# Kernel tuning notes

Hardware: AMD Instinct MI355X
Metric: run time of the kernel (lower is better)

Reference implementation:

```python
import jax, jax.numpy as jnp
import numpy as np

B, T, D, H, G = 256, 1024, 32, 64, 4 * 64  # batch, seq, input, hidden, gates


def setup_inputs() -> dict:
    key = jax.random.key(0)
    ks = jax.random.split(key, 12)
    s = 1.0 / np.sqrt(H)  # PyTorch LSTM default init scale
    return {
        "x": jax.random.normal(ks[0], (B, T, D), dtype=jnp.float32),
        "w_ih_l0": jax.random.normal(ks[1], (G, D), dtype=jnp.float32) * s,
        "w_hh_l0": jax.random.normal(ks[2], (G, H), dtype=jnp.float32) * s,
        "b_ih_l0": jax.random.normal(ks[3], (G,), dtype=jnp.float32) * s,
        "b_hh_l0": jax.random.normal(ks[4], (G,), dtype=jnp.float32) * s,
        "w_ih_l1": jax.random.normal(ks[5], (G, H), dtype=jnp.float32) * s,
        "w_hh_l1": jax.random.normal(ks[6], (G, H), dtype=jnp.float32) * s,
        "b_ih_l1": jax.random.normal(ks[7], (G,), dtype=jnp.float32) * s,
        "b_hh_l1": jax.random.normal(ks[8], (G,), dtype=jnp.float32) * s,
        "w_fc": jax.random.normal(ks[9], (1, H), dtype=jnp.float32) * s,
        "b_fc": jax.random.normal(ks[10], (1,), dtype=jnp.float32) * s,
    }


def _lstm_layer(x, w_ih, w_hh, b_ih, b_hh):
    """x: [B, T, Din] -> h_seq [B, T, H]. PyTorch gate order (i, f, g, o)."""
    # Precompute input contribution for all timesteps in one GEMM.
    gx = jnp.einsum('btd,gd->btg', x, w_ih) + b_ih + b_hh  # [B, T, 4H]
    gx = jnp.swapaxes(gx, 0, 1)  # [T, B, 4H] for scan over time
    h0 = jnp.zeros((x.shape[0], H), dtype=x.dtype)
    c0 = jnp.zeros((x.shape[0], H), dtype=x.dtype)

    def step(carry, g_t):
        h, c = carry
        g = g_t + h @ w_hh.T  # [B, 4H]
        i, f, gg, o = jnp.split(g, 4, axis=-1)
        i = jax.nn.sigmoid(i)
        f = jax.nn.sigmoid(f)
        gg = jnp.tanh(gg)
        o = jax.nn.sigmoid(o)
        c = f * c + i * gg
        h = o * jnp.tanh(c)
        return (h, c), h

    _, h_seq = jax.lax.scan(step, (h0, c0), gx)  # h_seq: [T, B, H]
    return jnp.swapaxes(h_seq, 0, 1)  # [B, T, H]


def reference(x, w_ih_l0, w_hh_l0, b_ih_l0, b_hh_l0,
              w_ih_l1, w_hh_l1, b_ih_l1, b_hh_l1, w_fc, b_fc):
    h1 = _lstm_layer(x, w_ih_l0, w_hh_l0, b_ih_l0, b_hh_l0)
    h2 = _lstm_layer(h1, w_ih_l1, w_hh_l1, b_ih_l1, b_hh_l1)
    last = h2[:, -1, :]  # [B, H]
    logits = last @ w_fc.T + b_fc  # [B, 1]
    return jax.nn.sigmoid(logits)
```

## Files before the change

kernel.cpp:

```cpp
#include <hip/hip_runtime.h>

#define TT 1024
#define DD 32
#define HH 64

typedef __fp16 h2v __attribute__((ext_vector_type(2)));
typedef _Float16 f16x8 __attribute__((ext_vector_type(8)));
typedef float f32x4 __attribute__((ext_vector_type(4)));

struct __attribute__((aligned(16))) H4 { h2v p[4]; };

__device__ __forceinline__ h2v pk(float a, float b) {
    return __builtin_amdgcn_cvt_pkrtz(a, b);
}
__device__ __forceinline__ float fsig(float x) {
    float e = __builtin_amdgcn_exp2f(-1.4426950408889634f * x);
    return __builtin_amdgcn_rcpf(1.0f + e);
}
__device__ __forceinline__ float ftanh(float x) {
    float e = __builtin_amdgcn_exp2f(2.885390081777927f * x);
    return 1.0f - 2.0f * __builtin_amdgcn_rcpf(1.0f + e);
}
__device__ __forceinline__ float pick4(f32x4 c, bool s0, bool s1) {
    float lo = s0 ? c[1] : c[0];
    float hi = s0 ? c[3] : c[2];
    return s1 ? hi : lo;
}
__device__ __forceinline__ f16x8 load_afrag(const float* p) {
    float4 f0 = *(const float4*)p;
    float4 f1 = *(const float4*)(p + 4);
    H4 t;
    t.p[0] = pk(f0.x, f0.y); t.p[1] = pk(f0.z, f0.w);
    t.p[2] = pk(f1.x, f1.y); t.p[3] = pk(f1.z, f1.w);
    return __builtin_bit_cast(f16x8, t);
}
#define MFMA16(A, B, C) __builtin_amdgcn_mfma_f32_16x16x32_f16(A, B, C, 0, 0, 0)

__global__ __launch_bounds__(512) void lstm2_b4(
    const float* __restrict__ x,
    const float* __restrict__ w_ih_l0, const float* __restrict__ w_hh_l0,
    const float* __restrict__ b_ih_l0, const float* __restrict__ b_hh_l0,
    const float* __restrict__ w_ih_l1, const float* __restrict__ w_hh_l1,
    const float* __restrict__ b_ih_l1, const float* __restrict__ b_hh_l1,
    const float* __restrict__ w_fc,   const float* __restrict__ b_fc,
    float* __restrict__ out)
{
    const int bbase = blockIdx.x * 4;
    const int tid  = threadIdx.x;
    const int wave = tid >> 6;
    const int lane = tid & 63;
    const bool isL1 = wave < 4;
    const int js   = wave & 3;
    const int quad = lane >> 4;
    const int bb   = lane & 3;
    const int rsel = (lane >> 2) & 3;
    const int jj   = js*16 + quad*4 + rsel;
    const int mrow = lane & 15;

    __shared__ __attribute__((aligned(16))) __fp16 buf[1280];

    {
        int* bi = (int*)buf;
        bi[tid] = 0;
        if (tid < 128) bi[512 + tid] = 0;
    }

    f16x8 A[16];
    float bs0, bs1, bs2, bs3;
    if (isL1) {
        #pragma unroll
        for (int q = 0; q < 4; ++q) {
            const int g = q*64 + js*16 + mrow;
            A[q*3 + 0] = load_afrag(w_ih_l0 + (size_t)g*DD + quad*8);
            A[q*3 + 1] = load_afrag(w_hh_l0 + (size_t)g*HH + quad*8);
            A[q*3 + 2] = load_afrag(w_hh_l0 + (size_t)g*HH + 32 + quad*8);
        }
        bs0 = b_ih_l0[0*64 + jj] + b_hh_l0[0*64 + jj];
        bs1 = b_ih_l0[1*64 + jj] + b_hh_l0[1*64 + jj];
        bs2 = b_ih_l0[2*64 + jj] + b_hh_l0[2*64 + jj];
        bs3 = b_ih_l0[3*64 + jj] + b_hh_l0[3*64 + jj];
    } else {
        #pragma unroll
        for (int q = 0; q < 4; ++q) {
            const int g = q*64 + js*16 + mrow;
            A[q*4 + 0] = load_afrag(w_ih_l1 + (size_t)g*HH + quad*8);
            A[q*4 + 1] = load_afrag(w_ih_l1 + (size_t)g*HH + 32 + quad*8);
            A[q*4 + 2] = load_afrag(w_hh_l1 + (size_t)g*HH + quad*8);
            A[q*4 + 3] = load_afrag(w_hh_l1 + (size_t)g*HH + 32 + quad*8);
        }
        bs0 = b_ih_l1[0*64 + jj] + b_hh_l1[0*64 + jj];
        bs1 = b_ih_l1[1*64 + jj] + b_hh_l1[1*64 + jj];
        bs2 = b_ih_l1[2*64 + jj] + b_hh_l1[2*64 + jj];
        bs3 = b_ih_l1[3*64 + jj] + b_hh_l1[3*64 + jj];
    }

    const int roff = (bb*4 + quad)*8;
    const int cw   = (isL1 ? 1 : 3) + (jj >> 5);
    const int woff = ((cw*4 + bb)*4 + ((jj & 31) >> 3))*8 + (jj & 7);

    const float* xg = x + (size_t)(bbase + (lane >> 4)) * (TT*DD) + (lane & 15)*2;
    const int sdw = ((lane >> 4)*4 + ((lane & 15) >> 2))*4 + ((lane & 15) & 3);
    float2 xv1 = {0.f, 0.f}, xv2 = {0.f, 0.f};

    __syncthreads();
    if (wave == 7) {
        float2 v0 = *(const float2*)xg;
        ((int*)buf)[sdw] = __builtin_bit_cast(int, pk(v0.x, v0.y));
        xv1 = *(const float2*)(xg + DD);
        xv2 = *(const float2*)(xg + 2*DD);
    }
    __syncthreads();

    const bool s0 = (rsel & 1) != 0;
    const bool s1 = (rsel & 2) != 0;
    float cst = 0.0f;

    for (int t = 0; t <= TT; ++t) {
        const int p = t & 1;
        const __fp16* bc = buf + p*640;
        __fp16* bn = buf + (p ^ 1)*640;
        if (isL1) {
            if (t < TT) {
                f16x8 B0 = *(const f16x8*)(bc + 0*128 + roff);
                f16x8 B1 = *(const f16x8*)(bc + 1*128 + roff);
                f16x8 B2 = *(const f16x8*)(bc + 2*128 + roff);

                f32x4 Z = {0.f, 0.f, 0.f, 0.f};
                f32x4 C0 = Z, C1 = Z, C2 = Z, C3 = Z;
                C0 = MFMA16(A[0], B0, C0); C0 = MFMA16(A[1],  B1, C0); C0 = MFMA16(A[2],  B2, C0);
                C1 = MFMA16(A[3], B0, C1); C1 = MFMA16(A[4],  B1, C1); C1 = MFMA16(A[5],  B2, C1);
                C2 = MFMA16(A[6], B0, C2); C2 = MFMA16(A[7],  B1, C2); C2 = MFMA16(A[8],  B2, C2);
                C3 = MFMA16(A[9], B0, C3); C3 = MFMA16(A[10], B1, C3); C3 = MFMA16(A[11], B2, C3);

                float Si = pick4(C0, s0, s1) + bs0;
                float Sf = pick4(C1, s0, s1) + bs1;
                float Sg = pick4(C2, s0, s1) + bs2;
                float So = pick4(C3, s0, s1) + bs3;

                float ii = fsig(Si), ff = fsig(Sf), oo = fsig(So);
                float gg = ftanh(Sg);
                cst = ff * cst + ii * gg;
                float hv = oo * ftanh(cst);
                bn[woff] = (__fp16)hv;
            }
        } else {
            if (wave == 7 && t < TT) {
                ((int*)bn)[sdw] = __builtin_bit_cast(int, pk(xv1.x, xv1.y));
                xv1 = xv2;
                const int tl = (t + 3 < TT) ? (t + 3) : (TT - 1);
                xv2 = *(const float2*)(xg + (size_t)tl*DD);
            }
            if (t > 0) {
                f16x8 B1 = *(const f16x8*)(bc + 1*128 + roff);
                f16x8 B2 = *(const f16x8*)(bc + 2*128 + roff);
                f16x8 B3 = *(const f16x8*)(bc + 3*128 + roff);
                f16x8 B4 = *(const f16x8*)(bc + 4*128 + roff);

                f32x4 Z = {0.f, 0.f, 0.f, 0.f};
                f32x4 C0 = Z, C1 = Z, C2 = Z, C3 = Z;
                C0 = MFMA16(A[0],  B1, C0); C0 = MFMA16(A[1],  B2, C0);
                C0 = MFMA16(A[2],  B3, C0); C0 = MFMA16(A[3],  B4, C0);
                C1 = MFMA16(A[4],  B1, C1); C1 = MFMA16(A[5],  B2, C1);
                C1 = MFMA16(A[6],  B3, C1); C1 = MFMA16(A[7],  B4, C1);
                C2 = MFMA16(A[8],  B1, C2); C2 = MFMA16(A[9],  B2, C2);
                C2 = MFMA16(A[10], B3, C2); C2 = MFMA16(A[11], B4, C2);
                C3 = MFMA16(A[12], B1, C3); C3 = MFMA16(A[13], B2, C3);
                C3 = MFMA16(A[14], B3, C3); C3 = MFMA16(A[15], B4, C3);

                float Si = pick4(C0, s0, s1) + bs0;
                float Sf = pick4(C1, s0, s1) + bs1;
                float Sg = pick4(C2, s0, s1) + bs2;
                float So = pick4(C3, s0, s1) + bs3;

                float ii = fsig(Si), ff = fsig(Sf), oo = fsig(So);
                float gg = ftanh(Sg);
                cst = ff * cst + ii * gg;
                float hv = oo * ftanh(cst);
                bn[woff] = (__fp16)hv;
            }
        }
        __syncthreads();
    }

    if (wave == 0) {
        const int jg = lane >> 2;
        float s = 0.f;
        #pragma unroll
        for (int u2 = 0; u2 < 4; ++u2) {
            const int j = jg*4 + u2;
            float hval = (float)buf[640 + (((3 + (j >> 5))*4 + bb)*4 + ((j & 31) >> 3))*8 + (j & 7)];
            s += hval * w_fc[j];
        }
        s += __shfl_xor(s, 4);
        s += __shfl_xor(s, 8);
        s += __shfl_xor(s, 16);
        s += __shfl_xor(s, 32);
        if (lane < 4) out[bbase + lane] = fsig(s + b_fc[0]);
    }
}

extern "C" void kernel_launch(void* const* d_in, const int* in_sizes, int n_in,
                              void* d_out, int out_size, void* d_ws, size_t ws_size,
                              hipStream_t stream) {
    lstm2_b4<<<dim3(64), dim3(512), 0, stream>>>(
        (const float*)d_in[0],
        (const float*)d_in[1], (const float*)d_in[2],
        (const float*)d_in[3], (const float*)d_in[4],
        (const float*)d_in[5], (const float*)d_in[6],
        (const float*)d_in[7], (const float*)d_in[8],
        (const float*)d_in[9], (const float*)d_in[10],
        (float*)d_out);
}
```

Measured before the change: 545.4 us.

## Feed x fragments straight from registers and split MFMA accumulation chains

Each layer-0 wave now loads its own x fragment from global memory into registers, with three timesteps prefetched, and packs it straight into the MFMA B operand. This drops the staging of x through shared memory by wave 7 and shrinks the LDS buffer. The dependent MFMA chains are split into two independent accumulators that are summed afterwards, to expose more instruction-level parallelism on the serial critical path. The per-step __syncthreads is replaced by an inline-asm LDS wait plus s_barrier, which avoids waiting on outstanding global loads. The cost is redundant global loads across the four layer-0 waves and extra registers.

```diff
diff --git a/kernel.cpp b/kernel.cpp
--- a/kernel.cpp
+++ b/kernel.cpp
@@ -20,23 +20,27 @@
 __device__ __forceinline__ float ftanh(float x) {
     float e = __builtin_amdgcn_exp2f(2.885390081777927f * x);
     return 1.0f - 2.0f * __builtin_amdgcn_rcpf(1.0f + e);
+}
+__device__ __forceinline__ void bar_lds() {
+    asm volatile("s_waitcnt lgkmcnt(0)\n\ts_barrier" ::: "memory");
 }
 __device__ __forceinline__ float pick4(f32x4 c, bool s0, bool s1) {
     float lo = s0 ? c[1] : c[0];
     float hi = s0 ? c[3] : c[2];
     return s1 ? hi : lo;
 }
+__device__ __forceinline__ f16x8 packx(float4 a, float4 b) {
+    H4 t;
+    t.p[0] = pk(a.x, a.y); t.p[1] = pk(a.z, a.w);
+    t.p[2] = pk(b.x, b.y); t.p[3] = pk(b.z, b.w);
+    return __builtin_bit_cast(f16x8, t);
+}
 __device__ __forceinline__ f16x8 load_afrag(const float* p) {
-    float4 f0 = *(const float4*)p;
-    float4 f1 = *(const float4*)(p + 4);
-    H4 t;
-    t.p[0] = pk(f0.x, f0.y); t.p[1] = pk(f0.z, f0.w);
-    t.p[2] = pk(f1.x, f1.y); t.p[3] = pk(f1.z, f1.w);
-    return __builtin_bit_cast(f16x8, t);
+    return packx(*(const float4*)p, *(const float4*)(p + 4));
 }
 #define MFMA16(A, B, C) __builtin_amdgcn_mfma_f32_16x16x32_f16(A, B, C, 0, 0, 0)
 
-__global__ __launch_bounds__(512) void lstm2_b4(
+__global__ __launch_bounds__(512) void lstm2_b4v2(
     const float* __restrict__ x,
     const float* __restrict__ w_ih_l0, const float* __restrict__ w_hh_l0,
     const float* __restrict__ b_ih_l0, const float* __restrict__ b_hh_l0,
@@ -57,13 +61,8 @@
     const int jj   = js*16 + quad*4 + rsel;
     const int mrow = lane & 15;
 
-    __shared__ __attribute__((aligned(16))) __fp16 buf[1280];
-
-    {
-        int* bi = (int*)buf;
-        bi[tid] = 0;
-        if (tid < 128) bi[512 + tid] = 0;
-    }
+    __shared__ __attribute__((aligned(16))) __fp16 buf[1024];
+    ((int*)buf)[tid] = 0;
 
     f16x8 A[16];
     float bs0, bs1, bs2, bs3;
@@ -95,47 +94,56 @@
     }
 
     const int roff = (bb*4 + quad)*8;
-    const int cw   = (isL1 ? 1 : 3) + (jj >> 5);
+    const int cw   = (isL1 ? 0 : 2) + (jj >> 5);
     const int woff = ((cw*4 + bb)*4 + ((jj & 31) >> 3))*8 + (jj & 7);
 
-    const float* xg = x + (size_t)(bbase + (lane >> 4)) * (TT*DD) + (lane & 15)*2;
-    const int sdw = ((lane >> 4)*4 + ((lane & 15) >> 2))*4 + ((lane & 15) & 3);
-    float2 xv1 = {0.f, 0.f}, xv2 = {0.f, 0.f};
-
-    __syncthreads();
-    if (wave == 7) {
-        float2 v0 = *(const float2*)xg;
-        ((int*)buf)[sdw] = __builtin_bit_cast(int, pk(v0.x, v0.y));
-        xv1 = *(const float2*)(xg + DD);
-        xv2 = *(const float2*)(xg + 2*DD);
-    }
+    const float* xg = x + (size_t)(bbase + bb) * (TT*DD) + quad*8;
+    float4 r0a, r0b, r1a, r1b, r2a, r2b;
+    if (isL1) {
+        r0a = *(const float4*)(xg);          r0b = *(const float4*)(xg + 4);
+        r1a = *(const float4*)(xg + DD);     r1b = *(const float4*)(xg + DD + 4);
+        r2a = *(const float4*)(xg + 2*DD);   r2b = *(const float4*)(xg + 2*DD + 4);
+    }
+
     __syncthreads();
 
     const bool s0 = (rsel & 1) != 0;
     const bool s1 = (rsel & 2) != 0;
     float cst = 0.0f;
+    const f32x4 Z = {0.f, 0.f, 0.f, 0.f};
 
     for (int t = 0; t <= TT; ++t) {
         const int p = t & 1;
-        const __fp16* bc = buf + p*640;
-        __fp16* bn = buf + (p ^ 1)*640;
+        const __fp16* bc = buf + p*512;
+        __fp16* bn = buf + (p ^ 1)*512;
         if (isL1) {
             if (t < TT) {
-                f16x8 B0 = *(const f16x8*)(bc + 0*128 + roff);
-                f16x8 B1 = *(const f16x8*)(bc + 1*128 + roff);
-                f16x8 B2 = *(const f16x8*)(bc + 2*128 + roff);
-
-                f32x4 Z = {0.f, 0.f, 0.f, 0.f};
-                f32x4 C0 = Z, C1 = Z, C2 = Z, C3 = Z;
-                C0 = MFMA16(A[0], B0, C0); C0 = MFMA16(A[1],  B1, C0); C0 = MFMA16(A[2],  B2, C0);
-                C1 = MFMA16(A[3], B0, C1); C1 = MFMA16(A[4],  B1, C1); C1 = MFMA16(A[5],  B2, C1);
-                C2 = MFMA16(A[6], B0, C2); C2 = MFMA16(A[7],  B1, C2); C2 = MFMA16(A[8],  B2, C2);
-                C3 = MFMA16(A[9], B0, C3); C3 = MFMA16(A[10], B1, C3); C3 = MFMA16(A[11], B2, C3);
-
-                float Si = pick4(C0, s0, s1) + bs0;
-                float Sf = pick4(C1, s0, s1) + bs1;
-                float Sg = pick4(C2, s0, s1) + bs2;
-                float So = pick4(C3, s0, s1) + bs3;
+                f16x8 Bx = packx(r0a, r0b);
+                r0a = r1a; r0b = r1b; r1a = r2a; r1b = r2b;
+                const int tl = (t + 3 < TT) ? (t + 3) : (TT - 1);
+                r2a = *(const float4*)(xg + (size_t)tl*DD);
+                r2b = *(const float4*)(xg + (size_t)tl*DD + 4);
+
+                f16x8 B1 = *(const f16x8*)(bc + 0*128 + roff);
+                f16x8 B2 = *(const f16x8*)(bc + 1*128 + roff);
+
+                f32x4 C0 = MFMA16(A[0], Bx, Z);
+                f32x4 C1 = MFMA16(A[3], Bx, Z);
+                f32x4 C2 = MFMA16(A[6], Bx, Z);
+                f32x4 C3 = MFMA16(A[9], Bx, Z);
+                C0 = MFMA16(A[1],  B1, C0);
+                C1 = MFMA16(A[4],  B1, C1);
+                C2 = MFMA16(A[7],  B1, C2);
+                C3 = MFMA16(A[10], B1, C3);
+                f32x4 D0 = MFMA16(A[2],  B2, Z);
+                f32x4 D1 = MFMA16(A[5],  B2, Z);
+                f32x4 D2 = MFMA16(A[8],  B2, Z);
+                f32x4 D3 = MFMA16(A[11], B2, Z);
+
+                float Si = pick4(C0, s0, s1) + pick4(D0, s0, s1) + bs0;
+                float Sf = pick4(C1, s0, s1) + pick4(D1, s0, s1) + bs1;
+                float Sg = pick4(C2, s0, s1) + pick4(D2, s0, s1) + bs2;
+                float So = pick4(C3, s0, s1) + pick4(D3, s0, s1) + bs3;
 
                 float ii = fsig(Si), ff = fsig(Sf), oo = fsig(So);
                 float gg = ftanh(Sg);
@@ -144,33 +152,25 @@
                 bn[woff] = (__fp16)hv;
             }
         } else {
-            if (wave == 7 && t < TT) {
-                ((int*)bn)[sdw] = __builtin_bit_cast(int, pk(xv1.x, xv1.y));
-                xv1 = xv2;
-                const int tl = (t + 3 < TT) ? (t + 3) : (TT - 1);
-                xv2 = *(const float2*)(xg + (size_t)tl*DD);
-            }
             if (t > 0) {
-                f16x8 B1 = *(const f16x8*)(bc + 1*128 + roff);
-                f16x8 B2 = *(const f16x8*)(bc + 2*128 + roff);
-                f16x8 B3 = *(const f16x8*)(bc + 3*128 + roff);
-                f16x8 B4 = *(const f16x8*)(bc + 4*128 + roff);
-
-                f32x4 Z = {0.f, 0.f, 0.f, 0.f};
-                f32x4 C0 = Z, C1 = Z, C2 = Z, C3 = Z;
-                C0 = MFMA16(A[0],  B1, C0); C0 = MFMA16(A[1],  B2, C0);
-                C0 = MFMA16(A[2],  B3, C0); C0 = MFMA16(A[3],  B4, C0);
-                C1 = MFMA16(A[4],  B1, C1); C1 = MFMA16(A[5],  B2, C1);
-                C1 = MFMA16(A[6],  B3, C1); C1 = MFMA16(A[7],  B4, C1);
-                C2 = MFMA16(A[8],  B1, C2); C2 = MFMA16(A[9],  B2, C2);
-                C2 = MFMA16(A[10], B3, C2); C2 = MFMA16(A[11], B4, C2);
-                C3 = MFMA16(A[12], B1, C3); C3 = MFMA16(A[13], B2, C3);
-                C3 = MFMA16(A[14], B3, C3); C3 = MFMA16(A[15], B4, C3);
-
-                float Si = pick4(C0, s0, s1) + bs0;
-                float Sf = pick4(C1, s0, s1) + bs1;
-                float Sg = pick4(C2, s0, s1) + bs2;
-                float So = pick4(C3, s0, s1) + bs3;
+                f16x8 B1 = *(const f16x8*)(bc + 0*128 + roff);
+                f16x8 B2 = *(const f16x8*)(bc + 1*128 + roff);
+                f16x8 B3 = *(const f16x8*)(bc + 2*128 + roff);
+                f16x8 B4 = *(const f16x8*)(bc + 3*128 + roff);
+
+                f32x4 C0 = MFMA16(A[0],  B1, Z); C0 = MFMA16(A[1],  B2, C0);
+                f32x4 C1 = MFMA16(A[4],  B1, Z); C1 = MFMA16(A[5],  B2, C1);
+                f32x4 C2 = MFMA16(A[8],  B1, Z); C2 = MFMA16(A[9],  B2, C2);
+                f32x4 C3 = MFMA16(A[12], B1, Z); C3 = MFMA16(A[13], B2, C3);
+                f32x4 D0 = MFMA16(A[2],  B3, Z); D0 = MFMA16(A[3],  B4, D0);
+                f32x4 D1 = MFMA16(A[6],  B3, Z); D1 = MFMA16(A[7],  B4, D1);
+                f32x4 D2 = MFMA16(A[10], B3, Z); D2 = MFMA16(A[11], B4, D2);
+                f32x4 D3 = MFMA16(A[14], B3, Z); D3 = MFMA16(A[15], B4, D3);
+
+                float Si = pick4(C0, s0, s1) + pick4(D0, s0, s1) + bs0;
+                float Sf = pick4(C1, s0, s1) + pick4(D1, s0, s1) + bs1;
+                float Sg = pick4(C2, s0, s1) + pick4(D2, s0, s1) + bs2;
+                float So = pick4(C3, s0, s1) + pick4(D3, s0, s1) + bs3;
 
                 float ii = fsig(Si), ff = fsig(Sf), oo = fsig(So);
                 float gg = ftanh(Sg);
@@ -179,7 +179,7 @@
                 bn[woff] = (__fp16)hv;
             }
         }
-        __syncthreads();
+        bar_lds();
     }
 
     if (wave == 0) {
@@ -188,7 +188,7 @@
         #pragma unroll
         for (int u2 = 0; u2 < 4; ++u2) {
             const int j = jg*4 + u2;
-            float hval = (float)buf[640 + (((3 + (j >> 5))*4 + bb)*4 + ((j & 31) >> 3))*8 + (j & 7)];
+            float hval = (float)buf[512 + (((2 + (j >> 5))*4 + bb)*4 + ((j & 31) >> 3))*8 + (j & 7)];
             s += hval * w_fc[j];
         }
         s += __shfl_xor(s, 4);
@@ -202,7 +202,7 @@
 extern "C" void kernel_launch(void* const* d_in, const int* in_sizes, int n_in,
                               void* d_out, int out_size, void* d_ws, size_t ws_size,
                               hipStream_t stream) {
-    lstm2_b4<<<dim3(64), dim3(512), 0, stream>>>(
+    lstm2_b4v2<<<dim3(64), dim3(512), 0, stream>>>(
         (const float*)d_in[0],
         (const float*)d_in[1], (const float*)d_in[2],
         (const float*)d_in[3], (const float*)d_in[4],
```

Measured after the change: 666.7 us. 22.2% more time.
